# Performance work log

Measured on AMD Instinct MI355X. Metric: run time of the kernel, lower is better.

Reference implementation:

```python
import jax, jax.numpy as jnp
import numpy as np

D_MODEL, N_HEADS, D_FF = 1024, 16, 4096
B, S = 2, 2048
EPS = 1e-6


def setup_inputs() -> dict:
    key = jax.random.key(0)
    ks = jax.random.split(key, 8)
    sc = 0.02
    x = jax.random.normal(ks[0], (B, S, D_MODEL), dtype=jnp.float32)
    Wq = jax.random.normal(ks[1], (D_MODEL, D_MODEL), dtype=jnp.float32) * sc
    Wk = jax.random.normal(ks[2], (D_MODEL, D_MODEL), dtype=jnp.float32) * sc
    Wv = jax.random.normal(ks[3], (D_MODEL, D_MODEL), dtype=jnp.float32) * sc
    Wo = jax.random.normal(ks[4], (D_MODEL, D_MODEL), dtype=jnp.float32) * sc
    W1 = jax.random.normal(ks[5], (D_MODEL, D_FF), dtype=jnp.float32) * sc
    W2 = jax.random.normal(ks[6], (D_FF, D_MODEL), dtype=jnp.float32) * sc
    z = lambda n: jnp.zeros((n,), dtype=jnp.float32)
    return {
        'x': x,
        'Wq': Wq, 'bq': z(D_MODEL), 'Wk': Wk, 'bk': z(D_MODEL),
        'Wv': Wv, 'bv': z(D_MODEL), 'Wo': Wo, 'bo': z(D_MODEL),
        'W1': W1, 'b1': z(D_FF), 'W2': W2, 'b2': z(D_MODEL),
        'alpha1': jnp.ones((D_MODEL,), jnp.float32), 'beta1': z(D_MODEL),
        'alpha2': jnp.ones((D_MODEL,), jnp.float32), 'beta2': z(D_MODEL),
    }


def _layernorm(y, alpha, beta):
    # torch.std is Bessel-corrected (N-1); original divides by (std + eps)
    d = y.shape[-1]
    m = jnp.mean(y, axis=-1, keepdims=True)
    c = y - m
    std = jnp.sqrt(jnp.sum(c * c, axis=-1, keepdims=True) / (d - 1))
    return alpha * c / (std + EPS) + beta


def reference(x, Wq, bq, Wk, bk, Wv, bv, Wo, bo, W1, b1, W2, b2,
              alpha1, beta1, alpha2, beta2):
    Bx, Sx, D = x.shape
    H = N_HEADS
    dk = D // H
    # projections -> [B, H, S, dk]
    q = (x @ Wq + bq).reshape(Bx, Sx, H, dk).transpose(0, 2, 1, 3)
    k = (x @ Wk + bk).reshape(Bx, Sx, H, dk).transpose(0, 2, 1, 3)
    v = (x @ Wv + bv).reshape(Bx, Sx, H, dk).transpose(0, 2, 1, 3)
    scores = jnp.einsum('bhqd,bhkd->bhqk', q, k) / np.sqrt(dk).astype(np.float32)
    attn = jax.nn.softmax(scores, axis=-1)  # [B, H, S, S]
    ctx = jnp.einsum('bhqk,bhkd->bhqd', attn, v)
    ctx = ctx.transpose(0, 2, 1, 3).reshape(Bx, Sx, D)
    attn_out = _layernorm(x + (ctx @ Wo + bo), alpha1, beta1)
    ff = jax.nn.relu(attn_out @ W1 + b1) @ W2 + b2
    enc_out = _layernorm(attn_out + ff, alpha2, beta2)
    return enc_out, attn
```

## Files before the change

kernel.cpp:

```cpp
#include <hip/hip_runtime.h>

typedef _Float16 h8 __attribute__((ext_vector_type(8)));
typedef _Float16 h4 __attribute__((ext_vector_type(4)));
typedef float f4 __attribute__((ext_vector_type(4)));
typedef unsigned short u16;
typedef unsigned short us8 __attribute__((ext_vector_type(8)));

#define MFMA16(a, b, c) __builtin_amdgcn_mfma_f32_16x16x32_f16(a, b, c, 0, 0, 0)

static __device__ __forceinline__ float bf2f(u16 u) {
  unsigned int x = ((unsigned int)u) << 16;
  return __builtin_bit_cast(float, x);
}
static __device__ __forceinline__ u16 f2bf(float f) {
  unsigned int x = __builtin_bit_cast(unsigned int, f);
  x += 0x7fffu + ((x >> 16) & 1u);
  return (u16)(x >> 16);
}

static __device__ __forceinline__ void gload16(const void* g, void* l) {
  __builtin_amdgcn_global_load_lds((const __attribute__((address_space(1))) void*)g,
                                   (__attribute__((address_space(3))) void*)l, 16, 0, 0);
}

__global__ void detect_dtype(const void* __restrict__ alpha1, int* __restrict__ flag) {
  u16 u = ((const u16*)alpha1)[0];
  *flag = (u == 0x3F80u) ? 1 : (u == 0x3C00u ? 2 : 0);
}

__global__ __launch_bounds__(256) void cvt_to_f16(const void* __restrict__ in,
                                                  _Float16* __restrict__ out, int n,
                                                  const int* __restrict__ flag) {
  int f = *flag;
  int i = (blockIdx.x * 256 + threadIdx.x) * 8;
  if (i >= n) return;
  h8 o;
  if (f == 1) {
    us8 v = *(const us8*)((const u16*)in + i);
#pragma unroll
    for (int j = 0; j < 8; ++j) o[j] = (_Float16)bf2f(v[j]);
  } else if (f == 0) {
    const float* p = (const float*)in + i;
    f4 a = *(const f4*)p;
    f4 b = *(const f4*)(p + 4);
#pragma unroll
    for (int j = 0; j < 4; ++j) {
      o[j] = (_Float16)a[j];
      o[4 + j] = (_Float16)b[j];
    }
  } else {
    o = *(const h8*)((const _Float16*)in + i);
  }
  *(h8*)(out + i) = o;
}

__global__ __launch_bounds__(256) void cvt_vecs(const void* v0, const void* v1, const void* v2,
                                                const void* v3, const void* v4, const void* v5,
                                                const void* v6, const void* v7, const void* v8,
                                                const void* v9, float* __restrict__ out,
                                                const int* __restrict__ flag) {
  int i = blockIdx.x * 256 + threadIdx.x;
  if (i >= 13312) return;
  const void* src;
  int off;
  if (i < 4096) {
    src = (i < 1024) ? v0 : (i < 2048) ? v1 : (i < 3072) ? v2 : v3;
    off = i & 1023;
  } else if (i < 8192) {
    src = v4;
    off = i - 4096;
  } else {
    int j = (i - 8192) >> 10;
    src = (j == 0) ? v5 : (j == 1) ? v6 : (j == 2) ? v7 : (j == 3) ? v8 : v9;
    off = i & 1023;
  }
  int f = *flag;
  float val = (f == 1)   ? bf2f(((const u16*)src)[off])
              : (f == 0) ? ((const float*)src)[off]
                         : (float)((const _Float16*)src)[off];
  out[i] = val;
}

__global__ __launch_bounds__(256) void transpose_any(const void* __restrict__ W,
                                                     _Float16* __restrict__ Wt, int K, int N,
                                                     const int* __restrict__ flag) {
  int f = *flag;
  __shared__ _Float16 t[32][33];
  int n0 = blockIdx.x * 32, k0 = blockIdx.y * 32;
  int tx = threadIdx.x, ty = threadIdx.y;
#pragma unroll
  for (int i = 0; i < 4; ++i) {
    size_t idx = (size_t)(k0 + ty + 8 * i) * N + n0 + tx;
    float v = (f == 1)   ? bf2f(((const u16*)W)[idx])
              : (f == 0) ? ((const float*)W)[idx]
                         : (float)((const _Float16*)W)[idx];
    t[ty + 8 * i][tx] = (_Float16)v;
  }
  __syncthreads();
#pragma unroll
  for (int i = 0; i < 4; ++i)
    Wt[(size_t)(n0 + ty + 8 * i) * K + k0 + tx] = t[tx][ty + 8 * i];
}

__global__ __launch_bounds__(256) void pack_qk(const _Float16* __restrict__ src,
                                               _Float16* __restrict__ dst, int coloff) {
  int id = blockIdx.x * 256 + threadIdx.x;
  int lane = id & 63, rest = id >> 6;
  int dt = rest & 1, st = (rest >> 1) & 127, bh = rest >> 8;
  int b = bh >> 4, h = bh & 15;
  int l15 = lane & 15, quad = lane >> 4;
  h8 v = *(const h8*)(src + (size_t)(b * 2048 + st * 16 + l15) * 3072 + coloff + h * 64 +
                      dt * 32 + quad * 8);
  *(h8*)(dst + (size_t)id * 8) = v;
}

__global__ __launch_bounds__(256) void pack_v(const _Float16* __restrict__ src,
                                              _Float16* __restrict__ dst) {
  __shared__ _Float16 t[32][72];
  int kt = blockIdx.x, bh = blockIdx.y;
  int b = bh >> 4, h = bh & 15;
  int tid = threadIdx.x;
  {
    int sl = tid >> 3, dp = (tid & 7) * 8;
    h8 v = *(const h8*)(src + (size_t)(b * 2048 + kt * 32 + sl) * 3072 + 2048 + h * 64 + dp);
    *(h8*)&t[sl][dp] = v;
  }
  __syncthreads();
  int nt = tid >> 6, lane = tid & 63;
  int l15 = lane & 15, quad = lane >> 4;
  h8 o;
#pragma unroll
  for (int j = 0; j < 8; ++j) o[j] = t[quad * 8 + j][nt * 16 + l15];
  *(h8*)(dst + (size_t)bh * 131072 + kt * 2048 + (size_t)tid * 8) = o;
}

#define F_RELU 1
#define F_RES 2

__global__ __launch_bounds__(256, 2) void gemm_bt(const _Float16* __restrict__ A,
                                                  const _Float16* __restrict__ Bt,
                                                  const float* __restrict__ bias,
                                                  const _Float16* __restrict__ resid,
                                                  _Float16* __restrict__ C, int M, int N, int K,
                                                  int flags) {
  __shared__ __align__(16) _Float16 As[2][128][32];
  __shared__ __align__(16) _Float16 Bs[2][128][32];
  const int tid = threadIdx.x;
  const int lane = tid & 63, wave = tid >> 6;
  const int quad = lane >> 4, l15 = lane & 15;
  const int m0 = blockIdx.y * 128, n0 = blockIdx.x * 128;
  const int wm = (wave >> 1) * 64, wn = (wave & 1) * 64;

  f4 acc[4][4] = {};

#define STAGE(buf, kk)                                                              \
  do {                                                                              \
    _Pragma("unroll") for (int c = 0; c < 2; ++c) {                                 \
      int id = c * 256 + tid;                                                       \
      int r = id >> 2, cc = id & 3;                                                 \
      gload16(A + (size_t)(m0 + r) * K + (kk) + cc * 8,                             \
              (char*)&As[buf][0][0] + c * 4096 + wave * 1024);                      \
      gload16(Bt + (size_t)(n0 + r) * K + (kk) + cc * 8,                            \
              (char*)&Bs[buf][0][0] + c * 4096 + wave * 1024);                      \
    }                                                                               \
  } while (0)

  STAGE(0, 0);
  __syncthreads();
  int cur = 0;
  for (int k0 = 0; k0 < K; k0 += 32) {
    if (k0 + 32 < K) STAGE(cur ^ 1, k0 + 32);
    h8 a[4], b[4];
#pragma unroll
    for (int i = 0; i < 4; ++i) a[i] = *(const h8*)&As[cur][wm + i * 16 + l15][quad * 8];
#pragma unroll
    for (int j = 0; j < 4; ++j) b[j] = *(const h8*)&Bs[cur][wn + j * 16 + l15][quad * 8];
#pragma unroll
    for (int i = 0; i < 4; ++i)
#pragma unroll
      for (int j = 0; j < 4; ++j) acc[i][j] = MFMA16(a[i], b[j], acc[i][j]);
    __syncthreads();
    cur ^= 1;
  }
#undef STAGE

#pragma unroll
  for (int j = 0; j < 4; ++j) {
    int col = n0 + wn + j * 16 + l15;
    float bi = bias[col];
#pragma unroll
    for (int i = 0; i < 4; ++i) {
      int rowb = m0 + wm + i * 16 + quad * 4;
#pragma unroll
      for (int r = 0; r < 4; ++r) {
        size_t off = (size_t)(rowb + r) * N + col;
        float v = acc[i][j][r] + bi;
        if (flags & F_RES) v += (float)resid[off];
        if (flags & F_RELU) v = fmaxf(v, 0.f);
        C[off] = (_Float16)v;
      }
    }
  }
}

__global__ __launch_bounds__(256, 2) void attn_kernel(const _Float16* __restrict__ Qf,
                                                      const _Float16* __restrict__ Kf,
                                                      const _Float16* __restrict__ Vf,
                                                      void* __restrict__ d_out_all,
                                                      _Float16* __restrict__ ctx,
                                                      const int* __restrict__ flag) {
  const int S = 2048, D = 1024;
  const int q0 = blockIdx.x * 16;
  const int h = blockIdx.y, b = blockIdx.z;
  const int bh = b * 16 + h;
  const int tid = threadIdx.x, lane = tid & 63, wave = tid >> 6;
  const int quad = lane >> 4, l15 = lane & 15;
  const float scale = 0.125f;
  const int f = *flag;

  const size_t fbase = (size_t)bh * 131072;
  const size_t eoff = 4194304ull + ((size_t)bh * S + q0) * S;
  float* of = (float*)d_out_all + eoff;
  u16* ob = (u16*)d_out_all + eoff;
  _Float16* oh = (_Float16*)d_out_all + eoff;

  h8 aq0 = *(const h8*)(Qf + fbase + (size_t)(q0 >> 4) * 1024 + lane * 8);
  h8 aq1 = *(const h8*)(Qf + fbase + (size_t)(q0 >> 4) * 1024 + 512 + lane * 8);

  __shared__ float sl[4][16];
  __shared__ __align__(16) _Float16 Ps[4][16][40];
  __shared__ float red[4][16][64];

  h4 pc[32];
  float l_acc[4] = {0.f, 0.f, 0.f, 0.f};
#pragma unroll
  for (int it = 0; it < 32; ++it) {
    int st = wave * 32 + it;
    h8 bk0 = *(const h8*)(Kf + fbase + (size_t)st * 1024 + lane * 8);
    h8 bk1 = *(const h8*)(Kf + fbase + (size_t)st * 1024 + 512 + lane * 8);
    f4 acc = {};
    acc = MFMA16(aq0, bk0, acc);
    acc = MFMA16(aq1, bk1, acc);
    h4 t;
#pragma unroll
    for (int r = 0; r < 4; ++r) {
      float e = __expf(acc[r] * scale);
      l_acc[r] += e;
      t[r] = (_Float16)e;
    }
    pc[it] = t;
  }
#pragma unroll
  for (int r = 0; r < 4; ++r) {
#pragma unroll
    for (int msk = 1; msk < 16; msk <<= 1) l_acc[r] += __shfl_xor(l_acc[r], msk);
  }
  if (l15 == 0) {
#pragma unroll
    for (int r = 0; r < 4; ++r) sl[wave][quad * 4 + r] = l_acc[r];
  }
  __syncthreads();
  float li[4];
#pragma unroll
  for (int r = 0; r < 4; ++r) {
    int row = quad * 4 + r;
    li[r] = 1.f / (sl[0][row] + sl[1][row] + sl[2][row] + sl[3][row]);
  }

  f4 accv[4] = {};
#pragma unroll
  for (int it2 = 0; it2 < 16; ++it2) {
    int k0 = wave * 512 + it2 * 32;
#pragma unroll
    for (int hh = 0; hh < 2; ++hh) {
      h4 t = pc[it2 * 2 + hh];
#pragma unroll
      for (int r = 0; r < 4; ++r) {
        float p = (float)t[r] * li[r];
        size_t aoff = (size_t)(quad * 4 + r) * S + k0 + hh * 16 + l15;
        if (f == 0)
          __builtin_nontemporal_store(p, &of[aoff]);
        else if (f == 1)
          __builtin_nontemporal_store(f2bf(p), &ob[aoff]);
        else
          __builtin_nontemporal_store((_Float16)p, &oh[aoff]);
        Ps[wave][quad * 4 + r][hh * 16 + l15] = (_Float16)p;
      }
    }
    h8 ap = *(const h8*)&Ps[wave][l15][quad * 8];
    int kt = k0 >> 5;
#pragma unroll
    for (int nt = 0; nt < 4; ++nt) {
      h8 bv = *(const h8*)(Vf + fbase + (size_t)kt * 2048 + nt * 512 + lane * 8);
      accv[nt] = MFMA16(ap, bv, accv[nt]);
    }
  }
#pragma unroll
  for (int nt = 0; nt < 4; ++nt)
#pragma unroll
    for (int r = 0; r < 4; ++r) red[wave][quad * 4 + r][nt * 16 + l15] = accv[nt][r];
  __syncthreads();
  const size_t cbase = (size_t)b * S * D + h * 64;
  for (int x = tid; x < 1024; x += 256) {
    int row = x >> 6, col = x & 63;
    float v = red[0][row][col] + red[1][row][col] + red[2][row][col] + red[3][row][col];
    ctx[cbase + (size_t)(q0 + row) * D + col] = (_Float16)v;
  }
}

__global__ __launch_bounds__(256) void layernorm_k(const _Float16* __restrict__ Y,
                                                   const float* __restrict__ alpha,
                                                   const float* __restrict__ beta,
                                                   _Float16* __restrict__ outh,
                                                   void* __restrict__ outv,
                                                   const int* __restrict__ flag) {
  const int D = 1024;
  int row = blockIdx.x, tid = threadIdx.x;
  int wave = tid >> 6, lane = tid & 63;
  const _Float16* y = Y + (size_t)row * D;
  float v[4], s = 0.f;
#pragma unroll
  for (int j = 0; j < 4; ++j) {
    v[j] = (float)y[tid + 256 * j];
    s += v[j];
  }
#pragma unroll
  for (int msk = 1; msk < 64; msk <<= 1) s += __shfl_xor(s, msk);
  __shared__ float rs[4];
  if (lane == 0) rs[wave] = s;
  __syncthreads();
  s = rs[0] + rs[1] + rs[2] + rs[3];
  float mean = s * (1.f / 1024.f);
  float ss = 0.f;
#pragma unroll
  for (int j = 0; j < 4; ++j) {
    v[j] -= mean;
    ss += v[j] * v[j];
  }
#pragma unroll
  for (int msk = 1; msk < 64; msk <<= 1) ss += __shfl_xor(ss, msk);
  __syncthreads();
  if (lane == 0) rs[wave] = ss;
  __syncthreads();
  ss = rs[0] + rs[1] + rs[2] + rs[3];
  float inv = 1.f / (sqrtf(ss * (1.f / 1023.f)) + 1e-6f);
  int f = flag ? *flag : 0;
#pragma unroll
  for (int j = 0; j < 4; ++j) {
    int col = tid + 256 * j;
    float o = alpha[col] * v[j] * inv + beta[col];
    size_t off = (size_t)row * D + col;
    if (outh) outh[off] = (_Float16)o;
    if (outv) {
      if (f == 0)
        ((float*)outv)[off] = o;
      else if (f == 1)
        ((u16*)outv)[off] = f2bf(o);
      else
        ((_Float16*)outv)[off] = (_Float16)o;
    }
  }
}

#define WS_ELEMS (61ull * 1048576ull)
__device__ __attribute__((aligned(256))) _Float16 g_fb[WS_ELEMS];

extern "C" void kernel_launch(void* const* d_in, const int* in_sizes, int n_in, void* d_out,
                              int out_size, void* d_ws, size_t ws_size, hipStream_t stream) {
  const void* x = d_in[0];
  const void* Wq = d_in[1];
  const void* bq = d_in[2];
  const void* Wk = d_in[3];
  const void* bk = d_in[4];
  const void* Wv = d_in[5];
  const void* bv = d_in[6];
  const void* Wo = d_in[7];
  const void* bo = d_in[8];
  const void* W1 = d_in[9];
  const void* b1 = d_in[10];
  const void* W2 = d_in[11];
  const void* b2 = d_in[12];
  const void* alpha1 = d_in[13];
  const void* beta1 = d_in[14];
  const void* alpha2 = d_in[15];
  const void* beta2 = d_in[16];

  _Float16* ws;
  if (ws_size >= WS_ELEMS * sizeof(_Float16)) {
    ws = (_Float16*)d_ws;
  } else {
    void* p = nullptr;
    hipGetSymbolAddress(&p, HIP_SYMBOL(g_fb));
    ws = (_Float16*)p;
  }
  const size_t MEG = 1048576;
  _Float16* xh = ws;
  _Float16* WqkvT = ws + 4 * MEG;
  _Float16* WoT = ws + 7 * MEG;
  _Float16* W1T = ws + 8 * MEG;
  _Float16* W2T = ws + 12 * MEG;
  _Float16* qkvh = ws + 16 * MEG;
  _Float16* Qf = ws + 28 * MEG;
  _Float16* Kf = ws + 32 * MEG;
  _Float16* Vf = ws + 36 * MEG;
  _Float16* ctxh = ws + 40 * MEG;
  _Float16* y1h = ws + 44 * MEG;
  _Float16* aoh = ws + 48 * MEG;
  _Float16* hh = ws + 16 * MEG;
  _Float16* y2h = ws + 52 * MEG;
  float* vecf = (float*)(ws + 60 * MEG);
  int* flag = (int*)(ws + 60 * MEG + 32768);

  const int BQ = 0, BO = 3072, B1 = 4096, B2 = 8192;
  const int A1 = 9216, BE1 = 10240, A2 = 11264, BE2 = 12288;

  detect_dtype<<<1, 1, 0, stream>>>(alpha1, flag);
  cvt_vecs<<<52, 256, 0, stream>>>(bq, bk, bv, bo, b1, b2, alpha1, beta1, alpha2, beta2, vecf,
                                   flag);
  cvt_to_f16<<<2048, 256, 0, stream>>>(x, xh, 4194304, flag);

  transpose_any<<<dim3(32, 32), dim3(32, 8), 0, stream>>>(Wq, WqkvT, 1024, 1024, flag);
  transpose_any<<<dim3(32, 32), dim3(32, 8), 0, stream>>>(Wk, WqkvT + 1024 * 1024, 1024, 1024,
                                                          flag);
  transpose_any<<<dim3(32, 32), dim3(32, 8), 0, stream>>>(Wv, WqkvT + 2 * 1024 * 1024, 1024,
                                                          1024, flag);
  transpose_any<<<dim3(32, 32), dim3(32, 8), 0, stream>>>(Wo, WoT, 1024, 1024, flag);
  transpose_any<<<dim3(128, 32), dim3(32, 8), 0, stream>>>(W1, W1T, 1024, 4096, flag);
  transpose_any<<<dim3(32, 128), dim3(32, 8), 0, stream>>>(W2, W2T, 4096, 1024, flag);

  gemm_bt<<<dim3(24, 32), 256, 0, stream>>>(xh, WqkvT, vecf + BQ, nullptr, qkvh, 4096, 3072,
                                            1024, 0);

  pack_qk<<<4096, 256, 0, stream>>>(qkvh, Qf, 0);
  pack_qk<<<4096, 256, 0, stream>>>(qkvh, Kf, 1024);
  pack_v<<<dim3(64, 32), 256, 0, stream>>>(qkvh, Vf);

  attn_kernel<<<dim3(128, 16, 2), 256, 0, stream>>>(Qf, Kf, Vf, d_out, ctxh, flag);

  gemm_bt<<<dim3(8, 32), 256, 0, stream>>>(ctxh, WoT, vecf + BO, xh, y1h, 4096, 1024, 1024,
                                           F_RES);
  layernorm_k<<<4096, 256, 0, stream>>>(y1h, vecf + A1, vecf + BE1, aoh, nullptr, flag);

  gemm_bt<<<dim3(32, 32), 256, 0, stream>>>(aoh, W1T, vecf + B1, nullptr, hh, 4096, 4096, 1024,
                                            F_RELU);
  gemm_bt<<<dim3(8, 32), 256, 0, stream>>>(hh, W2T, vecf + B2, aoh, y2h, 4096, 1024, 4096,
                                           F_RES);
  layernorm_k<<<4096, 256, 0, stream>>>(y2h, vecf + A2, vecf + BE2, nullptr, d_out, flag);
}
```

Measured before the change: 983.9 us.

## Deepen GEMM LDS pipeline with swizzle and widen attention query tiles

The GEMM moves from double to 4-stage LDS buffering. It uses explicit vmcnt waits and raw barriers, plus an XOR swizzle on LDS addresses to cut bank conflicts. The attention kernel now processes 64 queries per block instead of 16, so each K/V load is reused across four query tiles. Instead of caching exponentials in registers, it recomputes QK^T in a second pass. This trades extra MFMA and exp work for fewer K/V reloads and fewer blocks, while the larger LDS and register footprint may reduce occupancy.

```diff
diff --git a/kernel.cpp b/kernel.cpp
--- a/kernel.cpp
+++ b/kernel.cpp
@@ -143,8 +143,8 @@
                                                   const _Float16* __restrict__ resid,
                                                   _Float16* __restrict__ C, int M, int N, int K,
                                                   int flags) {
-  __shared__ __align__(16) _Float16 As[2][128][32];
-  __shared__ __align__(16) _Float16 Bs[2][128][32];
+  __shared__ __align__(16) _Float16 As[4][128][32];
+  __shared__ __align__(16) _Float16 Bs[4][128][32];
   const int tid = threadIdx.x;
   const int lane = tid & 63, wave = tid >> 6;
   const int quad = lane >> 4, l15 = lane & 15;
@@ -153,36 +153,71 @@
 
   f4 acc[4][4] = {};
 
-#define STAGE(buf, kk)                                                              \
-  do {                                                                              \
-    _Pragma("unroll") for (int c = 0; c < 2; ++c) {                                 \
-      int id = c * 256 + tid;                                                       \
-      int r = id >> 2, cc = id & 3;                                                 \
-      gload16(A + (size_t)(m0 + r) * K + (kk) + cc * 8,                             \
-              (char*)&As[buf][0][0] + c * 4096 + wave * 1024);                      \
-      gload16(Bt + (size_t)(n0 + r) * K + (kk) + cc * 8,                            \
-              (char*)&Bs[buf][0][0] + c * 4096 + wave * 1024);                      \
-    }                                                                               \
+  int r_s[2], cc_s[2];
+#pragma unroll
+  for (int c = 0; c < 2; ++c) {
+    int X = (c * 256 + tid) * 16;
+    int L = X ^ (((X >> 7) & 3) << 4);
+    r_s[c] = L >> 6;
+    cc_s[c] = (L >> 4) & 3;
+  }
+
+#define STAGE(buf, kk)                                                          \
+  do {                                                                          \
+    _Pragma("unroll") for (int c = 0; c < 2; ++c) {                             \
+      gload16(A + (size_t)(m0 + r_s[c]) * K + (kk) + cc_s[c] * 8,               \
+              (char*)As + (size_t)(buf)*8192 + c * 4096 + wave * 1024);         \
+      gload16(Bt + (size_t)(n0 + r_s[c]) * K + (kk) + cc_s[c] * 8,              \
+              (char*)Bs + (size_t)(buf)*8192 + c * 4096 + wave * 1024);         \
+    }                                                                           \
   } while (0)
 
+#define LDSA(buf, row) \
+  (*(const h8*)((const char*)As + (size_t)(buf)*8192 + (((row)*64 + quad * 16) ^ ((((row) >> 1) & 3) << 4))))
+#define LDSB(buf, row) \
+  (*(const h8*)((const char*)Bs + (size_t)(buf)*8192 + (((row)*64 + quad * 16) ^ ((((row) >> 1) & 3) << 4))))
+
+#define COMPUTE(buf)                                                            \
+  do {                                                                          \
+    h8 a[4], b[4];                                                              \
+    _Pragma("unroll") for (int i = 0; i < 4; ++i) a[i] = LDSA(buf, wm + i * 16 + l15); \
+    _Pragma("unroll") for (int j = 0; j < 4; ++j) b[j] = LDSB(buf, wn + j * 16 + l15); \
+    _Pragma("unroll") for (int i = 0; i < 4; ++i)                               \
+        _Pragma("unroll") for (int j = 0; j < 4; ++j) acc[i][j] =               \
+            MFMA16(a[i], b[j], acc[i][j]);                                      \
+  } while (0)
+
+#define SYNC(n)                                       \
+  do {                                                \
+    __builtin_amdgcn_sched_barrier(0);                \
+    asm volatile("s_waitcnt vmcnt(" #n ")" ::: "memory"); \
+    __builtin_amdgcn_s_barrier();                     \
+    __builtin_amdgcn_sched_barrier(0);                \
+  } while (0)
+
+  const int NT = K >> 5;
   STAGE(0, 0);
-  __syncthreads();
-  int cur = 0;
-  for (int k0 = 0; k0 < K; k0 += 32) {
-    if (k0 + 32 < K) STAGE(cur ^ 1, k0 + 32);
-    h8 a[4], b[4];
-#pragma unroll
-    for (int i = 0; i < 4; ++i) a[i] = *(const h8*)&As[cur][wm + i * 16 + l15][quad * 8];
-#pragma unroll
-    for (int j = 0; j < 4; ++j) b[j] = *(const h8*)&Bs[cur][wn + j * 16 + l15][quad * 8];
-#pragma unroll
-    for (int i = 0; i < 4; ++i)
-#pragma unroll
-      for (int j = 0; j < 4; ++j) acc[i][j] = MFMA16(a[i], b[j], acc[i][j]);
-    __syncthreads();
-    cur ^= 1;
-  }
+  STAGE(1, 32);
+  STAGE(2, 64);
+  SYNC(8);
+  int t = 0;
+  for (; t < NT - 3; ++t) {
+    STAGE((t + 3) & 3, (t + 3) * 32);
+    COMPUTE(t & 3);
+    SYNC(8);
+  }
+  COMPUTE(t & 3);
+  SYNC(4);
+  ++t;
+  COMPUTE(t & 3);
+  SYNC(0);
+  ++t;
+  COMPUTE(t & 3);
 #undef STAGE
+#undef LDSA
+#undef LDSB
+#undef COMPUTE
+#undef SYNC
 
 #pragma unroll
   for (int j = 0; j < 4; ++j) {
@@ -210,7 +245,7 @@
                                                       _Float16* __restrict__ ctx,
                                                       const int* __restrict__ flag) {
   const int S = 2048, D = 1024;
-  const int q0 = blockIdx.x * 16;
+  const int q0 = blockIdx.x * 64;
   const int h = blockIdx.y, b = blockIdx.z;
   const int bh = b * 16 + h;
   const int tid = threadIdx.x, lane = tid & 63, wave = tid >> 6;
@@ -224,87 +259,107 @@
   u16* ob = (u16*)d_out_all + eoff;
   _Float16* oh = (_Float16*)d_out_all + eoff;
 
-  h8 aq0 = *(const h8*)(Qf + fbase + (size_t)(q0 >> 4) * 1024 + lane * 8);
-  h8 aq1 = *(const h8*)(Qf + fbase + (size_t)(q0 >> 4) * 1024 + 512 + lane * 8);
-
-  __shared__ float sl[4][16];
-  __shared__ __align__(16) _Float16 Ps[4][16][40];
+  h8 aq[4][2];
+#pragma unroll
+  for (int t = 0; t < 4; ++t) {
+    aq[t][0] = *(const h8*)(Qf + fbase + (size_t)((q0 >> 4) + t) * 1024 + lane * 8);
+    aq[t][1] = *(const h8*)(Qf + fbase + (size_t)((q0 >> 4) + t) * 1024 + 512 + lane * 8);
+  }
+
+  __shared__ float sl[4][4][16];
+  __shared__ __align__(16) _Float16 Ps[4][4][16][40];
   __shared__ float red[4][16][64];
 
-  h4 pc[32];
-  float l_acc[4] = {0.f, 0.f, 0.f, 0.f};
-#pragma unroll
+  float l_acc[4][4] = {};
+#pragma unroll 4
   for (int it = 0; it < 32; ++it) {
     int st = wave * 32 + it;
     h8 bk0 = *(const h8*)(Kf + fbase + (size_t)st * 1024 + lane * 8);
     h8 bk1 = *(const h8*)(Kf + fbase + (size_t)st * 1024 + 512 + lane * 8);
-    f4 acc = {};
-    acc = MFMA16(aq0, bk0, acc);
-    acc = MFMA16(aq1, bk1, acc);
-    h4 t;
+#pragma unroll
+    for (int t = 0; t < 4; ++t) {
+      f4 s = {};
+      s = MFMA16(aq[t][0], bk0, s);
+      s = MFMA16(aq[t][1], bk1, s);
+#pragma unroll
+      for (int r = 0; r < 4; ++r) l_acc[t][r] += __expf(s[r] * scale);
+    }
+  }
+#pragma unroll
+  for (int t = 0; t < 4; ++t)
 #pragma unroll
     for (int r = 0; r < 4; ++r) {
-      float e = __expf(acc[r] * scale);
-      l_acc[r] += e;
-      t[r] = (_Float16)e;
-    }
-    pc[it] = t;
-  }
-#pragma unroll
-  for (int r = 0; r < 4; ++r) {
-#pragma unroll
-    for (int msk = 1; msk < 16; msk <<= 1) l_acc[r] += __shfl_xor(l_acc[r], msk);
-  }
+#pragma unroll
+      for (int msk = 1; msk < 16; msk <<= 1) l_acc[t][r] += __shfl_xor(l_acc[t][r], msk);
+    }
   if (l15 == 0) {
 #pragma unroll
-    for (int r = 0; r < 4; ++r) sl[wave][quad * 4 + r] = l_acc[r];
+    for (int t = 0; t < 4; ++t)
+#pragma unroll
+      for (int r = 0; r < 4; ++r) sl[wave][t][quad * 4 + r] = l_acc[t][r];
   }
   __syncthreads();
-  float li[4];
-#pragma unroll
-  for (int r = 0; r < 4; ++r) {
-    int row = quad * 4 + r;
-    li[r] = 1.f / (sl[0][row] + sl[1][row] + sl[2][row] + sl[3][row]);
-  }
-
-  f4 accv[4] = {};
-#pragma unroll
-  for (int it2 = 0; it2 < 16; ++it2) {
-    int k0 = wave * 512 + it2 * 32;
+  float li[4][4];
+#pragma unroll
+  for (int t = 0; t < 4; ++t)
+#pragma unroll
+    for (int r = 0; r < 4; ++r) {
+      int row = quad * 4 + r;
+      li[t][r] = 1.f / (sl[0][t][row] + sl[1][t][row] + sl[2][t][row] + sl[3][t][row]);
+    }
+
+  f4 accv[4][4] = {};
+  for (int it = 0; it < 16; ++it) {
+    int k0 = wave * 512 + it * 32;
+    int kt = k0 >> 5;
 #pragma unroll
     for (int hh = 0; hh < 2; ++hh) {
-      h4 t = pc[it2 * 2 + hh];
-#pragma unroll
-      for (int r = 0; r < 4; ++r) {
-        float p = (float)t[r] * li[r];
-        size_t aoff = (size_t)(quad * 4 + r) * S + k0 + hh * 16 + l15;
-        if (f == 0)
-          __builtin_nontemporal_store(p, &of[aoff]);
-        else if (f == 1)
-          __builtin_nontemporal_store(f2bf(p), &ob[aoff]);
-        else
-          __builtin_nontemporal_store((_Float16)p, &oh[aoff]);
-        Ps[wave][quad * 4 + r][hh * 16 + l15] = (_Float16)p;
+      int st = kt * 2 + hh;
+      h8 bk0 = *(const h8*)(Kf + fbase + (size_t)st * 1024 + lane * 8);
+      h8 bk1 = *(const h8*)(Kf + fbase + (size_t)st * 1024 + 512 + lane * 8);
+#pragma unroll
+      for (int t = 0; t < 4; ++t) {
+        f4 s = {};
+        s = MFMA16(aq[t][0], bk0, s);
+        s = MFMA16(aq[t][1], bk1, s);
+#pragma unroll
+        for (int r = 0; r < 4; ++r) {
+          float p = __expf(s[r] * scale) * li[t][r];
+          size_t aoff = (size_t)(t * 16 + quad * 4 + r) * S + k0 + hh * 16 + l15;
+          if (f == 0)
+            __builtin_nontemporal_store(p, &of[aoff]);
+          else if (f == 1)
+            __builtin_nontemporal_store(f2bf(p), &ob[aoff]);
+          else
+            __builtin_nontemporal_store((_Float16)p, &oh[aoff]);
+          Ps[wave][t][quad * 4 + r][hh * 16 + l15] = (_Float16)p;
+        }
       }
     }
-    h8 ap = *(const h8*)&Ps[wave][l15][quad * 8];
-    int kt = k0 >> 5;
+    h8 ap[4];
+#pragma unroll
+    for (int t = 0; t < 4; ++t) ap[t] = *(const h8*)&Ps[wave][t][l15][quad * 8];
 #pragma unroll
     for (int nt = 0; nt < 4; ++nt) {
       h8 bv = *(const h8*)(Vf + fbase + (size_t)kt * 2048 + nt * 512 + lane * 8);
-      accv[nt] = MFMA16(ap, bv, accv[nt]);
-    }
-  }
-#pragma unroll
-  for (int nt = 0; nt < 4; ++nt)
-#pragma unroll
-    for (int r = 0; r < 4; ++r) red[wave][quad * 4 + r][nt * 16 + l15] = accv[nt][r];
-  __syncthreads();
+#pragma unroll
+      for (int t = 0; t < 4; ++t) accv[t][nt] = MFMA16(ap[t], bv, accv[t][nt]);
+    }
+  }
   const size_t cbase = (size_t)b * S * D + h * 64;
-  for (int x = tid; x < 1024; x += 256) {
-    int row = x >> 6, col = x & 63;
-    float v = red[0][row][col] + red[1][row][col] + red[2][row][col] + red[3][row][col];
-    ctx[cbase + (size_t)(q0 + row) * D + col] = (_Float16)v;
+#pragma unroll 1
+  for (int t = 0; t < 4; ++t) {
+    if (t > 0) __syncthreads();
+#pragma unroll
+    for (int nt = 0; nt < 4; ++nt)
+#pragma unroll
+      for (int r = 0; r < 4; ++r) red[wave][quad * 4 + r][nt * 16 + l15] = accv[t][nt][r];
+    __syncthreads();
+    for (int x = tid; x < 1024; x += 256) {
+      int row = x >> 6, col = x & 63;
+      float v = red[0][row][col] + red[1][row][col] + red[2][row][col] + red[3][row][col];
+      ctx[cbase + (size_t)(q0 + t * 16 + row) * D + col] = (_Float16)v;
+    }
   }
 }
 
@@ -435,7 +490,7 @@
   pack_qk<<<4096, 256, 0, stream>>>(qkvh, Kf, 1024);
   pack_v<<<dim3(64, 32), 256, 0, stream>>>(qkvh, Vf);
 
-  attn_kernel<<<dim3(128, 16, 2), 256, 0, stream>>>(Qf, Kf, Vf, d_out, ctxh, flag);
+  attn_kernel<<<dim3(32, 16, 2), 256, 0, stream>>>(Qf, Kf, Vf, d_out, ctxh, flag);
 
   gemm_bt<<<dim3(8, 32), 256, 0, stream>>>(ctxh, WoT, vecf + BO, xh, y1h, 4096, 1024, 1024,
                                            F_RES);
```

Measured after the change: 1.064 ms. 1.08x slower.
